# Kernel tuning notes

Measured on AMD Instinct MI355X. Metric: run time of the kernel, lower is better.

## Reference

```python
import jax, jax.numpy as jnp
import numpy as np

EPS = 1e-6

def _linear_params(key, d_in, d_out):
    w = jax.random.normal(key, (d_in, d_out), dtype=jnp.float32) * np.sqrt(2.0 / (d_in + d_out))
    b = jnp.zeros((d_out,), dtype=jnp.float32)
    return w, b

def setup_inputs() -> dict:
    key = jax.random.key(0)
    ks = jax.random.split(key, 8)
    B, S, D = 4, 2048, 1024
    x = jax.random.normal(ks[0], (B, S, D), dtype=jnp.float32)
    wq, bq = _linear_params(ks[1], D, D)
    wk, bk = _linear_params(ks[2], D, D)
    wv, bv = _linear_params(ks[3], D, D)
    wo, bo = _linear_params(ks[4], D, D)
    w1, b1 = _linear_params(ks[5], D, D)
    w2, b2 = _linear_params(ks[6], D, D)
    g1 = jnp.ones((D,), jnp.float32); be1 = jnp.zeros((D,), jnp.float32)
    g2 = jnp.ones((D,), jnp.float32); be2 = jnp.zeros((D,), jnp.float32)
    return {"x": x, "wq": wq, "bq": bq, "wk": wk, "bk": bk, "wv": wv, "bv": bv,
            "wo": wo, "bo": bo, "w1": w1, "b1": b1, "w2": w2, "b2": b2,
            "g1": g1, "be1": be1, "g2": g2, "be2": be2}

def _layernorm(x, gamma, beta):
    mean = jnp.mean(x, axis=-1, keepdims=True)
    # torch .std() default is unbiased (ddof=1); eps added to std (not var)
    std = jnp.std(x, axis=-1, keepdims=True, ddof=1)
    return gamma * (x - mean) / (std + EPS) + beta

def _attention(x, wq, bq, wk, bk, wv, bv, wo, bo):
    S = x.shape[-2]
    q = x @ wq + bq  # [B,S,D]
    k = x @ wk + bk
    v = x @ wv + bv
    scores = jnp.einsum('bsd,btd->bst', q, k) / jnp.sqrt(jnp.asarray(S, jnp.float32))
    causal = jnp.tril(jnp.ones((S, S), dtype=bool))  # keep lower triangle incl. diag
    scores = jnp.where(causal, scores, -jnp.inf)
    attn = jax.nn.softmax(scores, axis=-1)
    out = jnp.einsum('bst,btd->bsd', attn, v)
    return out @ wo + bo

def reference(x, wq, bq, wk, bk, wv, bv, wo, bo, w1, b1, w2, b2, g1, be1, g2, be2):
    h = _attention(_layernorm(x, g1, be1), wq, bq, wk, bk, wv, bv, wo, bo) + x
    m = _layernorm(h, g2, be2)
    m = jnp.maximum(m @ w1 + b1, 0.0) @ w2 + b2
    return m + h
```

## Files before the change

### kernel.cpp

```cpp
#include <hip/hip_runtime.h>
#include <math.h>

#define BB 4
#define SS 2048
#define DD 1024
#define MM (BB*SS)
#define SD ((size_t)SS*DD)
#define MD ((size_t)MM*DD)
#define PPB ((size_t)2162688)

#define WT_OFF (3*MD + 4*PPB)
#define ZP_OFF (WT_OFF + 6*(size_t)DD*DD)
#define REQ_WS ((ZP_OFF + 16) * 2)

constexpr float LN_EPS = 1e-6f;

typedef __attribute__((ext_vector_type(8))) __bf16 bf16x8;
typedef __attribute__((ext_vector_type(4))) float f32x4;

__device__ __forceinline__ unsigned short f2bfbits(float f){
    unsigned u = __float_as_uint(f);
    u += 0x7FFFu + ((u >> 16) & 1u);
    return (unsigned short)(u >> 16);
}
__device__ __forceinline__ int rowWidth(int s){ return ((s >> 6) + 1) << 6; }
__device__ __forceinline__ size_t rowOff(int s){
    int g = s >> 6;
    return (size_t)4096 * (size_t)((g * (g + 1)) >> 1) + (size_t)(s & 63) * (size_t)((g + 1) << 6);
}
__device__ __forceinline__ void gl_lds(const unsigned short* g, unsigned short* l){
    __builtin_amdgcn_global_load_lds(
        (const __attribute__((address_space(1))) unsigned int*)g,
        (__attribute__((address_space(3))) unsigned int*)l, 16, 0, 0);
}

__device__ __forceinline__ int3 xcd_swz(){
    const int gx = gridDim.x, gy = gridDim.y, gz = gridDim.z;
    const int n = gx * gy * gz;
    int lin = blockIdx.x + gx * (blockIdx.y + gy * blockIdx.z);
    const int cpx = n >> 3;
    lin = (lin & 7) * cpx + (lin >> 3);
    int3 r;
    r.x = lin % gx; lin /= gx;
    r.y = lin % gy;
    r.z = lin / gy;
    return r;
}

__global__ __launch_bounds__(256)
void sentinel_kernel(float* __restrict__ out, const float val){
    out[(size_t)blockIdx.x * 256 + threadIdx.x] = val;
}

struct WPack { const float* w[6]; unsigned short* o[6]; unsigned short* zp; };
__global__ __launch_bounds__(256)
void wtrans(WPack wp)
{
    __shared__ float Ts[64][65];
    const float* W = wp.w[blockIdx.z];
    unsigned short* WT = wp.o[blockIdx.z];
    const int r0 = blockIdx.y*64, c0 = blockIdx.x*64;
    const int tid = threadIdx.x;
    if (blockIdx.x == 0 && blockIdx.y == 0 && blockIdx.z == 0 && tid < 16) wp.zp[tid] = 0;
    #pragma unroll
    for (int i = 0; i < 16; ++i){
        int lin = tid + i*256;
        int r = lin >> 6, c = lin & 63;
        Ts[r][c] = W[(size_t)(r0+r)*DD + c0+c];
    }
    __syncthreads();
    #pragma unroll
    for (int i = 0; i < 16; ++i){
        int lin = tid + i*256;
        int r = lin >> 6, c = lin & 63;
        WT[(size_t)(c0+r)*DD + r0+c] = f2bfbits(Ts[c][r]);
    }
}

__global__ __launch_bounds__(256)
void ln_f32(const float* __restrict__ x, const float* __restrict__ gamma,
            const float* __restrict__ beta, unsigned short* __restrict__ out)
{
    __shared__ float red[4];
    const int row = blockIdx.x;
    const int tid = threadIdx.x;
    float4 xv = ((const float4*)(x + (size_t)row*DD))[tid];
    float v[4] = {xv.x, xv.y, xv.z, xv.w};
    float s = v[0]+v[1]+v[2]+v[3];
    #pragma unroll
    for (int off = 32; off > 0; off >>= 1) s += __shfl_down(s, off, 64);
    if ((tid & 63) == 0) red[tid >> 6] = s;
    __syncthreads();
    const float mean = (red[0]+red[1]+red[2]+red[3]) * (1.0f/DD);
    __syncthreads();
    float q = 0.f;
    #pragma unroll
    for (int i = 0; i < 4; ++i){ float d = v[i]-mean; q += d*d; }
    #pragma unroll
    for (int off = 32; off > 0; off >>= 1) q += __shfl_down(q, off, 64);
    if ((tid & 63) == 0) red[tid >> 6] = q;
    __syncthreads();
    const float var = (red[0]+red[1]+red[2]+red[3]) * (1.0f/(DD-1));
    const float inv = 1.0f/(sqrtf(var) + LN_EPS);
    float4 g4 = ((const float4*)gamma)[tid];
    float4 b4 = ((const float4*)beta)[tid];
    ushort4 o;
    o.x = f2bfbits(g4.x*(v[0]-mean)*inv + b4.x);
    o.y = f2bfbits(g4.y*(v[1]-mean)*inv + b4.y);
    o.z = f2bfbits(g4.z*(v[2]-mean)*inv + b4.z);
    o.w = f2bfbits(g4.w*(v[3]-mean)*inv + b4.w);
    ((ushort4*)(out + (size_t)row*DD))[tid] = o;
}

template<bool RELU, bool RES, bool OUTF, bool BIAS_M>
__device__ __forceinline__ void gemm_core8(
    const unsigned short* __restrict__ A, const unsigned short* __restrict__ B,
    const float* __restrict__ bias, const float* __restrict__ resF,
    unsigned short* __restrict__ outB, float* __restrict__ outF,
    const int N, const int K, const int lda, const int ldb,
    const int m0, const int n0, unsigned short* S)
{
    unsigned short* A0 = S;
    unsigned short* A1 = S + 16384;
    unsigned short* A2 = S + 32768;
    unsigned short* B0 = S + 49152;
    unsigned short* B1 = S + 57344;
    unsigned short* B2 = S + 65536;

    const int tid = threadIdx.x, lane = tid & 63, wave = tid >> 6;
    const int wr = (wave >> 1) * 64;
    const int wc = (wave & 1) * 64;
    const int quad = lane >> 4, l15 = lane & 15;

    const unsigned short* ga[4]; const unsigned short* gb[2];
    #pragma unroll
    for (int c = 0; c < 4; ++c){
        const int mr = (wave*4 + c)*8 + (lane >> 3);
        const int gk = ((lane & 7) - mr) & 7;
        ga[c] = A + (size_t)(m0 + mr)*lda + gk*8;
    }
    #pragma unroll
    for (int c = 0; c < 2; ++c){
        const int mr = (wave*2 + c)*8 + (lane >> 3);
        const int gk = ((lane & 7) - mr) & 7;
        gb[c] = B + (size_t)(n0 + mr)*ldb + gk*8;
    }

    f32x4 acc[4][4] = {};
    const int NT = K >> 6;

    #pragma unroll
    for (int c = 0; c < 4; ++c) gl_lds(ga[c], &A0[(wave*4+c)*512]);
    #pragma unroll
    for (int c = 0; c < 2; ++c) gl_lds(gb[c], &B0[(wave*2+c)*512]);
    #pragma unroll
    for (int c = 0; c < 4; ++c) gl_lds(ga[c] + 64, &A1[(wave*4+c)*512]);
    #pragma unroll
    for (int c = 0; c < 2; ++c) gl_lds(gb[c] + 64, &B1[(wave*2+c)*512]);
    asm volatile("s_waitcnt vmcnt(6)" ::: "memory");
    __builtin_amdgcn_s_barrier();

    for (int t = 0; t < NT; ++t){
        const int kn = (t + 2) << 6;
        const bool more2 = (t + 2 < NT);
        #pragma unroll
        for (int kk = 0; kk < 2; ++kk){
            bf16x8 af[4], bfr[4];
            #pragma unroll
            for (int u = 0; u < 4; ++u){
                const int ra = wr + u*16 + l15, rb = wc + u*16 + l15, gi = kk*4 + quad;
                af[u]  = *(const bf16x8*)&A0[ra*64 + (((gi + ra) & 7) << 3)];
                bfr[u] = *(const bf16x8*)&B0[rb*64 + (((gi + rb) & 7) << 3)];
            }
            if (kk == 0 && more2){
                #pragma unroll
                for (int c = 0; c < 4; ++c) gl_lds(ga[c] + kn, &A2[(wave*4+c)*512]);
                #pragma unroll
                for (int c = 0; c < 2; ++c) gl_lds(gb[c] + kn, &B2[(wave*2+c)*512]);
            }
            __builtin_amdgcn_s_barrier();
            asm volatile("s_waitcnt lgkmcnt(0)" ::: "memory");
            __builtin_amdgcn_sched_barrier(0);
            __builtin_amdgcn_s_setprio(1);
            #pragma unroll
            for (int i = 0; i < 4; ++i)
                #pragma unroll
                for (int j = 0; j < 4; ++j)
                    acc[i][j] = __builtin_amdgcn_mfma_f32_16x16x32_bf16(af[i], bfr[j], acc[i][j], 0, 0, 0);
            __builtin_amdgcn_s_setprio(0);
            if (kk == 1){
                if (more2) asm volatile("s_waitcnt vmcnt(6)" ::: "memory");
                else       asm volatile("s_waitcnt vmcnt(0)" ::: "memory");
            }
            __builtin_amdgcn_s_barrier();
        }
        unsigned short* ta = A0; A0 = A1; A1 = A2; A2 = ta;
        unsigned short* tb = B0; B0 = B1; B1 = B2; B2 = tb;
    }

    #pragma unroll
    for (int i = 0; i < 4; ++i){
        #pragma unroll
        for (int r = 0; r < 4; ++r){
            const int m = m0 + wr + i*16 + quad*4 + r;
            const float bm = BIAS_M ? bias[m] : 0.f;
            #pragma unroll
            for (int j = 0; j < 4; ++j){
                const int n = n0 + wc + j*16 + l15;
                float v = acc[i][j][r] + (BIAS_M ? bm : bias[n]);
                if constexpr (RELU) v = fmaxf(v, 0.f);
                if constexpr (RES) v += resF[(size_t)m*N + n];
                if constexpr (OUTF) outF[(size_t)m*N + n] = v;
                else outB[(size_t)m*N + n] = f2bfbits(v);
            }
        }
    }
}

template<bool RELU, bool RES, bool OUTF, bool BIAS_M>
__global__ __launch_bounds__(512)
void gemm_mfma(const unsigned short* __restrict__ A, const unsigned short* __restrict__ B,
               const float* __restrict__ bias, const float* __restrict__ resF,
               unsigned short* __restrict__ outB, float* __restrict__ outF,
               const int N, const int K, const int lda, const int ldb)
{
    __shared__ unsigned short Smem[73728];
    const int3 b = xcd_swz();
    gemm_core8<RELU,RES,OUTF,BIAS_M>(A, B, bias, resF, outB, outF, N, K, lda, ldb,
                                     b.y*256, b.x*128, Smem);
}

__global__ __launch_bounds__(512)
void gemm_qk(const unsigned short* __restrict__ LN,
             const unsigned short* __restrict__ WqT, const unsigned short* __restrict__ WkT,
             const float* __restrict__ bq, const float* __restrict__ bk,
             unsigned short* __restrict__ Qw, unsigned short* __restrict__ Kw)
{
    __shared__ unsigned short Smem[73728];
    const int3 b = xcd_swz();
    const bool isK = (b.z != 0);
    gemm_core8<false,false,false,false>(LN, isK ? WkT : WqT, isK ? bk : bq, nullptr,
                                        isK ? Kw : Qw, nullptr, DD, DD, DD, DD,
                                        b.y*256, b.x*128, Smem);
}

__global__ __launch_bounds__(256)
void scores_mfma(const unsigned short* __restrict__ Qb, const unsigned short* __restrict__ Kb,
                 unsigned short* __restrict__ Pb, const float scale)
{
    const int3 b = xcd_swz();
    const int s0 = b.y*128, t0 = b.x*128;
    if (t0 > s0) return;
    const unsigned short* Q  = Qb + (size_t)b.z*SD;
    const unsigned short* Km = Kb + (size_t)b.z*SD;
    unsigned short* P        = Pb + (size_t)b.z*PPB;
    __shared__ unsigned short As[128*64];
    __shared__ unsigned short Bs[128*64];
    const int tid = threadIdx.x, lane = tid & 63, wave = tid >> 6;
    const int wm = ((wave >> 1) & 1) * 64, wn = (wave & 1) * 64;
    const int quad = lane >> 4, l15 = lane & 15;
    const unsigned short* ga[4]; const unsigned short* gb[4];
    #pragma unroll
    for (int c = 0; c < 4; ++c){
        const int mr = (wave*4 + c)*8 + (lane >> 3);
        const int gk = ((lane & 7) - mr) & 7;
        ga[c] = Q  + (size_t)(s0 + mr)*DD + gk*8;
        gb[c] = Km + (size_t)(t0 + mr)*DD + gk*8;
    }
    f32x4 acc[4][4] = {};
    for (int k0 = 0; k0 < DD; k0 += 64){
        #pragma unroll
        for (int c = 0; c < 4; ++c){
            gl_lds(ga[c] + k0, &As[(wave*4+c)*512]);
            gl_lds(gb[c] + k0, &Bs[(wave*4+c)*512]);
        }
        __syncthreads();
        #pragma unroll
        for (int kk = 0; kk < 2; ++kk){
            bf16x8 af[4], bfr[4];
            #pragma unroll
            for (int t = 0; t < 4; ++t){
                const int ra = wm + t*16 + l15, rb = wn + t*16 + l15, gi = kk*4 + quad;
                af[t]  = *(const bf16x8*)&As[ra*64 + (((gi + ra) & 7) << 3)];
                bfr[t] = *(const bf16x8*)&Bs[rb*64 + (((gi + rb) & 7) << 3)];
            }
            #pragma unroll
            for (int i = 0; i < 4; ++i)
                #pragma unroll
                for (int j = 0; j < 4; ++j)
                    acc[i][j] = __builtin_amdgcn_mfma_f32_16x16x32_bf16(af[i], bfr[j], acc[i][j], 0, 0, 0);
        }
        __syncthreads();
    }
    #pragma unroll
    for (int i = 0; i < 4; ++i){
        #pragma unroll
        for (int r = 0; r < 4; ++r){
            const int s = s0 + wm + i*16 + quad*4 + r;
            const int width = rowWidth(s);
            unsigned short* pr = P + rowOff(s);
            #pragma unroll
            for (int j = 0; j < 4; ++j){
                const int t = t0 + wn + j*16 + l15;
                if (t < width) pr[t] = f2bfbits(acc[i][j][r] * scale);
            }
        }
    }
}

__global__ __launch_bounds__(256)
void softmax_p(unsigned short* __restrict__ Pb)
{
    __shared__ float red[4];
    const int s = blockIdx.x;
    const int width = rowWidth(s);
    unsigned short* r = Pb + (size_t)blockIdx.y * PPB + rowOff(s);
    const int tid = threadIdx.x;
    float vals[8];
    float m = -1e30f;
    #pragma unroll
    for (int i = 0; i < 8; ++i){
        int t = tid + i*256;
        float v = -1e30f;
        if (t <= s) v = __uint_as_float(((unsigned)r[t]) << 16);
        vals[i] = v; m = fmaxf(m, v);
    }
    #pragma unroll
    for (int off = 32; off > 0; off >>= 1) m = fmaxf(m, __shfl_down(m, off, 64));
    if ((tid & 63) == 0) red[tid >> 6] = m;
    __syncthreads();
    const float M4 = fmaxf(fmaxf(red[0],red[1]), fmaxf(red[2],red[3]));
    __syncthreads();
    float ev[8]; float sum = 0.f;
    #pragma unroll
    for (int i = 0; i < 8; ++i){ ev[i] = __expf(vals[i] - M4); sum += ev[i]; }
    #pragma unroll
    for (int off = 32; off > 0; off >>= 1) sum += __shfl_down(sum, off, 64);
    if ((tid & 63) == 0) red[tid >> 6] = sum;
    __syncthreads();
    const float inv = 1.0f / (red[0]+red[1]+red[2]+red[3]);
    #pragma unroll
    for (int i = 0; i < 8; ++i){
        int t = tid + i*256;
        if (t < width) r[t] = f2bfbits(ev[i] * inv);
    }
}

__global__ __launch_bounds__(256)
void pv_mfma(const unsigned short* __restrict__ Pb, const unsigned short* __restrict__ VT,
             unsigned short* __restrict__ Cb, const unsigned short* __restrict__ zpad)
{
    const int3 b = xcd_swz();
    const int s0 = b.y*128, n0 = b.x*128;
    const unsigned short* P = Pb + (size_t)b.z*PPB;
    unsigned short* C       = Cb + (size_t)b.z*SD;
    const int bcol = b.z*SS;
    __shared__ unsigned short As[128*64];
    __shared__ unsigned short Bs[128*64];
    const int tid = threadIdx.x, lane = tid & 63, wave = tid >> 6;
    const int wm = ((wave >> 1) & 1) * 64, wn = (wave & 1) * 64;
    const int quad = lane >> 4, l15 = lane & 15;
    const unsigned short* ga[4]; const unsigned short* gb[4]; int pw[4];
    #pragma unroll
    for (int c = 0; c < 4; ++c){
        const int mr = (wave*4 + c)*8 + (lane >> 3);
        const int gk = ((lane & 7) - mr) & 7;
        const int s = s0 + mr;
        pw[c] = rowWidth(s) - gk*8;
        ga[c] = P + rowOff(s) + gk*8;
        gb[c] = VT + (size_t)(n0 + mr)*MM + bcol + gk*8;
    }
    f32x4 acc[4][4] = {};
    const int kmax = s0 + 128;
    for (int k0 = 0; k0 < kmax; k0 += 64){
        #pragma unroll
        for (int c = 0; c < 4; ++c){
            const unsigned short* gp = (k0 < pw[c]) ? (ga[c] + k0) : zpad;
            gl_lds(gp, &As[(wave*4+c)*512]);
            gl_lds(gb[c] + k0, &Bs[(wave*4+c)*512]);
        }
        __syncthreads();
        #pragma unroll
        for (int kk = 0; kk < 2; ++kk){
            bf16x8 af[4], bfr[4];
            #pragma unroll
            for (int t = 0; t < 4; ++t){
                const int ra = wm + t*16 + l15, rb = wn + t*16 + l15, gi = kk*4 + quad;
                af[t]  = *(const bf16x8*)&As[ra*64 + (((gi + ra) & 7) << 3)];
                bfr[t] = *(const bf16x8*)&Bs[rb*64 + (((gi + rb) & 7) << 3)];
            }
            #pragma unroll
            for (int i = 0; i < 4; ++i)
                #pragma unroll
                for (int j = 0; j < 4; ++j)
                    acc[i][j] = __builtin_amdgcn_mfma_f32_16x16x32_bf16(af[i], bfr[j], acc[i][j], 0, 0, 0);
        }
        __syncthreads();
    }
    #pragma unroll
    for (int i = 0; i < 4; ++i){
        #pragma unroll
        for (int r = 0; r < 4; ++r){
            const int s = s0 + wm + i*16 + quad*4 + r;
            #pragma unroll
            for (int j = 0; j < 4; ++j){
                const int n = n0 + wn + j*16 + l15;
                C[(size_t)s*DD + n] = f2bfbits(acc[i][j][r]);
            }
        }
    }
}

extern "C" void kernel_launch(void* const* d_in, const int* in_sizes, int n_in,
                              void* d_out, int out_size, void* d_ws, size_t ws_size,
                              hipStream_t stream)
{
    (void)in_sizes; (void)n_in; (void)out_size;
    const float* x   = (const float*)d_in[0];
    const float* bq  = (const float*)d_in[2];
    const float* bk  = (const float*)d_in[4];
    const float* bv  = (const float*)d_in[6];
    const float* bo  = (const float*)d_in[8];
    const float* b1  = (const float*)d_in[10];
    const float* b2  = (const float*)d_in[12];
    const float* g1  = (const float*)d_in[13];
    const float* be1 = (const float*)d_in[14];
    const float* g2  = (const float*)d_in[15];
    const float* be2 = (const float*)d_in[16];
    float* outf = (float*)d_out;

    if (ws_size < (size_t)REQ_WS){
        sentinel_kernel<<<dim3((unsigned)(MD/256)), dim3(256), 0, stream>>>(outf, 1.0e9f);
        return;
    }

    unsigned short* wsb = (unsigned short*)d_ws;
    unsigned short* Qw  = wsb;
    unsigned short* Kw  = wsb + MD;
    unsigned short* VTw = wsb + 2*MD;
    unsigned short* Pw  = wsb + 3*MD;
    unsigned short* WT  = wsb + WT_OFF;
    unsigned short* ZP  = wsb + ZP_OFF;
    float*          Hf  = (float*)Kw;
    unsigned short* CTX = Qw;
    unsigned short* MIDw= Pw;
    unsigned short* LN  = (unsigned short*)d_out;

    WPack wp;
    static const int widx[6] = {1,3,5,7,9,11};
    for (int i = 0; i < 6; ++i){
        wp.w[i] = (const float*)d_in[widx[i]];
        wp.o[i] = WT + (size_t)i*DD*DD;
    }
    wp.zp = ZP;
    unsigned short* WqT = wp.o[0]; unsigned short* WkT = wp.o[1];
    unsigned short* WvT = wp.o[2]; unsigned short* WoT = wp.o[3];
    unsigned short* W1T = wp.o[4]; unsigned short* W2T = wp.o[5];

    const dim3 blk(256);
    const dim3 blk8(512);
    const float scale = 1.0f / sqrtf((float)SS);
    const dim3 gA8(DD/128, MM/256);
    const dim3 gVT8(MM/128, DD/256);

    wtrans<<<dim3(16,16,6), blk, 0, stream>>>(wp);
    ln_f32<<<dim3(MM), blk, 0, stream>>>(x, g1, be1, LN);
    gemm_qk<<<dim3(DD/128, MM/256, 2), blk8, 0, stream>>>(LN, WqT, WkT, bq, bk, Qw, Kw);
    gemm_mfma<false,false,false,true ><<<gVT8, blk8, 0, stream>>>(WvT, LN, bv, nullptr, VTw, nullptr, MM, DD, DD, DD);
    scores_mfma<<<dim3(SS/128, SS/128, BB), blk, 0, stream>>>(Qw, Kw, Pw, scale);
    softmax_p<<<dim3(SS, BB), blk, 0, stream>>>(Pw);
    pv_mfma<<<dim3(DD/128, SS/128, BB), blk, 0, stream>>>(Pw, VTw, CTX, ZP);
    gemm_mfma<false,true,true,false><<<gA8, blk8, 0, stream>>>(CTX, WoT, bo, x, nullptr, Hf, DD, DD, DD, DD);
    ln_f32<<<dim3(MM), blk, 0, stream>>>(Hf, g2, be2, LN);
    gemm_mfma<true,false,false,false><<<gA8, blk8, 0, stream>>>(LN, W1T, b1, nullptr, MIDw, nullptr, DD, DD, DD, DD);
    gemm_mfma<false,true,true,false><<<gA8, blk8, 0, stream>>>(MIDw, W2T, b2, Hf, nullptr, outf, DD, DD, DD, DD);
}
```

Baseline: 375.0 us.

## Reuse triple-buffered 256x128 GEMM loop for causal scores and PV kernels

The pipelined GEMM main loop is factored into a shared routine with an optional packed/zero-padded A operand. The scores and PV kernels now use it: 512 threads, 256x128 tiles and triple-buffered async global-to-LDS loads, replacing their single-buffered loops that synchronised twice per K step. The aim is to overlap loads with MFMA work and raise per-block reuse in the attention GEMMs. In exchange, causal tiles get coarser, so more work above the diagonal is computed and then masked or read as zero padding, and fewer blocks are launched.

```diff
diff --git a/kernel.cpp b/kernel.cpp
--- a/kernel.cpp
+++ b/kernel.cpp
@@ -112,13 +112,12 @@
     ((ushort4*)(out + (size_t)row*DD))[tid] = o;
 }
 
-template<bool RELU, bool RES, bool OUTF, bool BIAS_M>
-__device__ __forceinline__ void gemm_core8(
-    const unsigned short* __restrict__ A, const unsigned short* __restrict__ B,
-    const float* __restrict__ bias, const float* __restrict__ resF,
-    unsigned short* __restrict__ outB, float* __restrict__ outF,
-    const int N, const int K, const int lda, const int ldb,
-    const int m0, const int n0, unsigned short* S)
+template<bool PACKED_A>
+__device__ __forceinline__ void gemm_loop8(
+    const unsigned short* const ga[4], const unsigned short* const gb[2],
+    const int* pw, const unsigned short* zpad,
+    const int NT, unsigned short* S, f32x4 acc[4][4],
+    const int wave, const int lane)
 {
     unsigned short* A0 = S;
     unsigned short* A1 = S + 16384;
@@ -127,36 +126,25 @@
     unsigned short* B1 = S + 57344;
     unsigned short* B2 = S + 65536;
 
-    const int tid = threadIdx.x, lane = tid & 63, wave = tid >> 6;
+    const int quad = lane >> 4, l15 = lane & 15;
     const int wr = (wave >> 1) * 64;
     const int wc = (wave & 1) * 64;
-    const int quad = lane >> 4, l15 = lane & 15;
-
-    const unsigned short* ga[4]; const unsigned short* gb[2];
-    #pragma unroll
-    for (int c = 0; c < 4; ++c){
-        const int mr = (wave*4 + c)*8 + (lane >> 3);
-        const int gk = ((lane & 7) - mr) & 7;
-        ga[c] = A + (size_t)(m0 + mr)*lda + gk*8;
-    }
-    #pragma unroll
-    for (int c = 0; c < 2; ++c){
-        const int mr = (wave*2 + c)*8 + (lane >> 3);
-        const int gk = ((lane & 7) - mr) & 7;
-        gb[c] = B + (size_t)(n0 + mr)*ldb + gk*8;
-    }
-
-    f32x4 acc[4][4] = {};
-    const int NT = K >> 6;
-
-    #pragma unroll
-    for (int c = 0; c < 4; ++c) gl_lds(ga[c], &A0[(wave*4+c)*512]);
-    #pragma unroll
-    for (int c = 0; c < 2; ++c) gl_lds(gb[c], &B0[(wave*2+c)*512]);
-    #pragma unroll
-    for (int c = 0; c < 4; ++c) gl_lds(ga[c] + 64, &A1[(wave*4+c)*512]);
-    #pragma unroll
-    for (int c = 0; c < 2; ++c) gl_lds(gb[c] + 64, &B1[(wave*2+c)*512]);
+
+    auto stageA = [&](unsigned short* buf, int koff){
+        #pragma unroll
+        for (int c = 0; c < 4; ++c){
+            const unsigned short* gp = ga[c] + koff;
+            if constexpr (PACKED_A) { if (koff >= pw[c]) gp = zpad; }
+            gl_lds(gp, &buf[(wave*4+c)*512]);
+        }
+    };
+    auto stageB = [&](unsigned short* buf, int koff){
+        #pragma unroll
+        for (int c = 0; c < 2; ++c) gl_lds(gb[c] + koff, &buf[(wave*2+c)*512]);
+    };
+
+    stageA(A0, 0);  stageB(B0, 0);
+    stageA(A1, 64); stageB(B1, 64);
     asm volatile("s_waitcnt vmcnt(6)" ::: "memory");
     __builtin_amdgcn_s_barrier();
 
@@ -173,10 +161,7 @@
                 bfr[u] = *(const bf16x8*)&B0[rb*64 + (((gi + rb) & 7) << 3)];
             }
             if (kk == 0 && more2){
-                #pragma unroll
-                for (int c = 0; c < 4; ++c) gl_lds(ga[c] + kn, &A2[(wave*4+c)*512]);
-                #pragma unroll
-                for (int c = 0; c < 2; ++c) gl_lds(gb[c] + kn, &B2[(wave*2+c)*512]);
+                stageA(A2, kn); stageB(B2, kn);
             }
             __builtin_amdgcn_s_barrier();
             asm volatile("s_waitcnt lgkmcnt(0)" ::: "memory");
@@ -197,7 +182,46 @@
         unsigned short* ta = A0; A0 = A1; A1 = A2; A2 = ta;
         unsigned short* tb = B0; B0 = B1; B1 = B2; B2 = tb;
     }
-
+}
+
+__device__ __forceinline__ void mk_ga(const unsigned short* base, size_t ld, int r0,
+                                      int wave, int lane, const unsigned short* ga[4]){
+    #pragma unroll
+    for (int c = 0; c < 4; ++c){
+        const int mr = (wave*4 + c)*8 + (lane >> 3);
+        const int gk = ((lane & 7) - mr) & 7;
+        ga[c] = base + (size_t)(r0 + mr)*ld + gk*8;
+    }
+}
+__device__ __forceinline__ void mk_gb(const unsigned short* base, size_t ld, int r0,
+                                      int wave, int lane, const unsigned short* gb[2]){
+    #pragma unroll
+    for (int c = 0; c < 2; ++c){
+        const int mr = (wave*2 + c)*8 + (lane >> 3);
+        const int gk = ((lane & 7) - mr) & 7;
+        gb[c] = base + (size_t)(r0 + mr)*ld + gk*8;
+    }
+}
+
+template<bool RELU, bool RES, bool OUTF, bool BIAS_M>
+__global__ __launch_bounds__(512)
+void gemm_mfma(const unsigned short* __restrict__ A, const unsigned short* __restrict__ B,
+               const float* __restrict__ bias, const float* __restrict__ resF,
+               unsigned short* __restrict__ outB, float* __restrict__ outF,
+               const int N, const int K, const int lda, const int ldb)
+{
+    __shared__ unsigned short Smem[73728];
+    const int3 b = xcd_swz();
+    const int m0 = b.y*256, n0 = b.x*128;
+    const int tid = threadIdx.x, lane = tid & 63, wave = tid >> 6;
+    const unsigned short* ga[4]; const unsigned short* gb[2];
+    mk_ga(A, lda, m0, wave, lane, ga);
+    mk_gb(B, ldb, n0, wave, lane, gb);
+    f32x4 acc[4][4] = {};
+    gemm_loop8<false>(ga, gb, nullptr, nullptr, K >> 6, Smem, acc, wave, lane);
+
+    const int quad = lane >> 4, l15 = lane & 15;
+    const int wr = (wave >> 1) * 64, wc = (wave & 1) * 64;
     #pragma unroll
     for (int i = 0; i < 4; ++i){
         #pragma unroll
@@ -217,19 +241,6 @@
     }
 }
 
-template<bool RELU, bool RES, bool OUTF, bool BIAS_M>
-__global__ __launch_bounds__(512)
-void gemm_mfma(const unsigned short* __restrict__ A, const unsigned short* __restrict__ B,
-               const float* __restrict__ bias, const float* __restrict__ resF,
-               unsigned short* __restrict__ outB, float* __restrict__ outF,
-               const int N, const int K, const int lda, const int ldb)
-{
-    __shared__ unsigned short Smem[73728];
-    const int3 b = xcd_swz();
-    gemm_core8<RELU,RES,OUTF,BIAS_M>(A, B, bias, resF, outB, outF, N, K, lda, ldb,
-                                     b.y*256, b.x*128, Smem);
-}
-
 __global__ __launch_bounds__(512)
 void gemm_qk(const unsigned short* __restrict__ LN,
              const unsigned short* __restrict__ WqT, const unsigned short* __restrict__ WkT,
@@ -239,69 +250,63 @@
     __shared__ unsigned short Smem[73728];
     const int3 b = xcd_swz();
     const bool isK = (b.z != 0);
-    gemm_core8<false,false,false,false>(LN, isK ? WkT : WqT, isK ? bk : bq, nullptr,
-                                        isK ? Kw : Qw, nullptr, DD, DD, DD, DD,
-                                        b.y*256, b.x*128, Smem);
-}
-
-__global__ __launch_bounds__(256)
+    const unsigned short* Bw = isK ? WkT : WqT;
+    const float* bias = isK ? bk : bq;
+    unsigned short* out = isK ? Kw : Qw;
+    const int m0 = b.y*256, n0 = b.x*128;
+    const int tid = threadIdx.x, lane = tid & 63, wave = tid >> 6;
+    const unsigned short* ga[4]; const unsigned short* gb[2];
+    mk_ga(LN, DD, m0, wave, lane, ga);
+    mk_gb(Bw, DD, n0, wave, lane, gb);
+    f32x4 acc[4][4] = {};
+    gemm_loop8<false>(ga, gb, nullptr, nullptr, DD >> 6, Smem, acc, wave, lane);
+
+    const int quad = lane >> 4, l15 = lane & 15;
+    const int wr = (wave >> 1) * 64, wc = (wave & 1) * 64;
+    #pragma unroll
+    for (int i = 0; i < 4; ++i){
+        #pragma unroll
+        for (int r = 0; r < 4; ++r){
+            const int m = m0 + wr + i*16 + quad*4 + r;
+            #pragma unroll
+            for (int j = 0; j < 4; ++j){
+                const int n = n0 + wc + j*16 + l15;
+                out[(size_t)m*DD + n] = f2bfbits(acc[i][j][r] + bias[n]);
+            }
+        }
+    }
+}
+
+__global__ __launch_bounds__(512)
 void scores_mfma(const unsigned short* __restrict__ Qb, const unsigned short* __restrict__ Kb,
                  unsigned short* __restrict__ Pb, const float scale)
 {
     const int3 b = xcd_swz();
-    const int s0 = b.y*128, t0 = b.x*128;
-    if (t0 > s0) return;
+    const int s0 = b.y*256, t0 = b.x*128;
+    if (t0 >= s0 + 256) return;
     const unsigned short* Q  = Qb + (size_t)b.z*SD;
     const unsigned short* Km = Kb + (size_t)b.z*SD;
     unsigned short* P        = Pb + (size_t)b.z*PPB;
-    __shared__ unsigned short As[128*64];
-    __shared__ unsigned short Bs[128*64];
+    __shared__ unsigned short Smem[73728];
     const int tid = threadIdx.x, lane = tid & 63, wave = tid >> 6;
-    const int wm = ((wave >> 1) & 1) * 64, wn = (wave & 1) * 64;
+    const unsigned short* ga[4]; const unsigned short* gb[2];
+    mk_ga(Q,  DD, s0, wave, lane, ga);
+    mk_gb(Km, DD, t0, wave, lane, gb);
+    f32x4 acc[4][4] = {};
+    gemm_loop8<false>(ga, gb, nullptr, nullptr, DD >> 6, Smem, acc, wave, lane);
+
     const int quad = lane >> 4, l15 = lane & 15;
-    const unsigned short* ga[4]; const unsigned short* gb[4];
-    #pragma unroll
-    for (int c = 0; c < 4; ++c){
-        const int mr = (wave*4 + c)*8 + (lane >> 3);
-        const int gk = ((lane & 7) - mr) & 7;
-        ga[c] = Q  + (size_t)(s0 + mr)*DD + gk*8;
-        gb[c] = Km + (size_t)(t0 + mr)*DD + gk*8;
-    }
-    f32x4 acc[4][4] = {};
-    for (int k0 = 0; k0 < DD; k0 += 64){
-        #pragma unroll
-        for (int c = 0; c < 4; ++c){
-            gl_lds(ga[c] + k0, &As[(wave*4+c)*512]);
-            gl_lds(gb[c] + k0, &Bs[(wave*4+c)*512]);
-        }
-        __syncthreads();
-        #pragma unroll
-        for (int kk = 0; kk < 2; ++kk){
-            bf16x8 af[4], bfr[4];
-            #pragma unroll
-            for (int t = 0; t < 4; ++t){
-                const int ra = wm + t*16 + l15, rb = wn + t*16 + l15, gi = kk*4 + quad;
-                af[t]  = *(const bf16x8*)&As[ra*64 + (((gi + ra) & 7) << 3)];
-                bfr[t] = *(const bf16x8*)&Bs[rb*64 + (((gi + rb) & 7) << 3)];
-            }
-            #pragma unroll
-            for (int i = 0; i < 4; ++i)
-                #pragma unroll
-                for (int j = 0; j < 4; ++j)
-                    acc[i][j] = __builtin_amdgcn_mfma_f32_16x16x32_bf16(af[i], bfr[j], acc[i][j], 0, 0, 0);
-        }
-        __syncthreads();
-    }
+    const int wr = (wave >> 1) * 64, wc = (wave & 1) * 64;
     #pragma unroll
     for (int i = 0; i < 4; ++i){
         #pragma unroll
         for (int r = 0; r < 4; ++r){
-            const int s = s0 + wm + i*16 + quad*4 + r;
+            const int s = s0 + wr + i*16 + quad*4 + r;
             const int width = rowWidth(s);
             unsigned short* pr = P + rowOff(s);
             #pragma unroll
             for (int j = 0; j < 4; ++j){
-                const int t = t0 + wn + j*16 + l15;
+                const int t = t0 + wc + j*16 + l15;
                 if (t < width) pr[t] = f2bfbits(acc[i][j][r] * scale);
             }
         }
@@ -346,21 +351,18 @@
     }
 }
 
-__global__ __launch_bounds__(256)
+__global__ __launch_bounds__(512)
 void pv_mfma(const unsigned short* __restrict__ Pb, const unsigned short* __restrict__ VT,
              unsigned short* __restrict__ Cb, const unsigned short* __restrict__ zpad)
 {
     const int3 b = xcd_swz();
-    const int s0 = b.y*128, n0 = b.x*128;
+    const int s0 = b.y*256, n0 = b.x*128;
     const unsigned short* P = Pb + (size_t)b.z*PPB;
     unsigned short* C       = Cb + (size_t)b.z*SD;
     const int bcol = b.z*SS;
-    __shared__ unsigned short As[128*64];
-    __shared__ unsigned short Bs[128*64];
+    __shared__ unsigned short Smem[73728];
     const int tid = threadIdx.x, lane = tid & 63, wave = tid >> 6;
-    const int wm = ((wave >> 1) & 1) * 64, wn = (wave & 1) * 64;
-    const int quad = lane >> 4, l15 = lane & 15;
-    const unsigned short* ga[4]; const unsigned short* gb[4]; int pw[4];
+    const unsigned short* ga[4]; const unsigned short* gb[2]; int pw[4];
     #pragma unroll
     for (int c = 0; c < 4; ++c){
         const int mr = (wave*4 + c)*8 + (lane >> 3);
@@ -368,43 +370,27 @@
         const int s = s0 + mr;
         pw[c] = rowWidth(s) - gk*8;
         ga[c] = P + rowOff(s) + gk*8;
+    }
+    #pragma unroll
+    for (int c = 0; c < 2; ++c){
+        const int mr = (wave*2 + c)*8 + (lane >> 3);
+        const int gk = ((lane & 7) - mr) & 7;
         gb[c] = VT + (size_t)(n0 + mr)*MM + bcol + gk*8;
     }
     f32x4 acc[4][4] = {};
-    const int kmax = s0 + 128;
-    for (int k0 = 0; k0 < kmax; k0 += 64){
-        #pragma unroll
-        for (int c = 0; c < 4; ++c){
-            const unsigned short* gp = (k0 < pw[c]) ? (ga[c] + k0) : zpad;
-            gl_lds(gp, &As[(wave*4+c)*512]);
-            gl_lds(gb[c] + k0, &Bs[(wave*4+c)*512]);
-        }
-        __syncthreads();
-        #pragma unroll
-        for (int kk = 0; kk < 2; ++kk){
-            bf16x8 af[4], bfr[4];
-            #pragma unroll
-            for (int t = 0; t < 4; ++t){
-                const int ra = wm + t*16 + l15, rb = wn + t*16 + l15, gi = kk*4 + quad;
-                af[t]  = *(const bf16x8*)&As[ra*64 + (((gi + ra) & 7) << 3)];
-                bfr[t] = *(const bf16x8*)&Bs[rb*64 + (((gi + rb) & 7) << 3)];
-            }
-            #pragma unroll
-            for (int i = 0; i < 4; ++i)
-                #pragma unroll
-                for (int j = 0; j < 4; ++j)
-                    acc[i][j] = __builtin_amdgcn_mfma_f32_16x16x32_bf16(af[i], bfr[j], acc[i][j], 0, 0, 0);
-        }
-        __syncthreads();
-    }
+    const int NT = (s0 + 256) >> 6;
+    gemm_loop8<true>(ga, gb, pw, zpad, NT, Smem, acc, wave, lane);
+
+    const int quad = lane >> 4, l15 = lane & 15;
+    const int wr = (wave >> 1) * 64, wc = (wave & 1) * 64;
     #pragma unroll
     for (int i = 0; i < 4; ++i){
         #pragma unroll
         for (int r = 0; r < 4; ++r){
-            const int s = s0 + wm + i*16 + quad*4 + r;
+            const int s = s0 + wr + i*16 + quad*4 + r;
             #pragma unroll
             for (int j = 0; j < 4; ++j){
-                const int n = n0 + wn + j*16 + l15;
+                const int n = n0 + wc + j*16 + l15;
                 C[(size_t)s*DD + n] = f2bfbits(acc[i][j][r]);
             }
         }
@@ -467,9 +453,9 @@
     ln_f32<<<dim3(MM), blk, 0, stream>>>(x, g1, be1, LN);
     gemm_qk<<<dim3(DD/128, MM/256, 2), blk8, 0, stream>>>(LN, WqT, WkT, bq, bk, Qw, Kw);
     gemm_mfma<false,false,false,true ><<<gVT8, blk8, 0, stream>>>(WvT, LN, bv, nullptr, VTw, nullptr, MM, DD, DD, DD);
-    scores_mfma<<<dim3(SS/128, SS/128, BB), blk, 0, stream>>>(Qw, Kw, Pw, scale);
+    scores_mfma<<<dim3(SS/128, SS/256, BB), blk8, 0, stream>>>(Qw, Kw, Pw, scale);
     softmax_p<<<dim3(SS, BB), blk, 0, stream>>>(Pw);
-    pv_mfma<<<dim3(DD/128, SS/128, BB), blk, 0, stream>>>(Pw, VTw, CTX, ZP);
+    pv_mfma<<<dim3(DD/128, SS/256, BB), blk8, 0, stream>>>(Pw, VTw, CTX, ZP);
     gemm_mfma<false,true,true,false><<<gA8, blk8, 0, stream>>>(CTX, WoT, bo, x, nullptr, Hf, DD, DD, DD, DD);
     ln_f32<<<dim3(MM), blk, 0, stream>>>(Hf, g2, be2, LN);
     gemm_mfma<true,false,false,false><<<gA8, blk8, 0, stream>>>(LN, W1T, b1, nullptr, MIDw, nullptr, DD, DD, DD, DD);
```

New measurement: 376.2 us. Within noise of the previous version (+0.3%).
